# Kernel tuning notes

Hardware: AMD Instinct MI355X
Metric: run time of the kernel (lower is better)

The kernel has to match this reference:

```python
import jax, jax.numpy as jnp
import numpy as np

N_NODES = 2048


def setup_inputs() -> dict:
    key = jax.random.key(0)
    ks = jax.random.split(key, 9)
    N, IN, HID, OUT, R, B1 = N_NODES, 64, 32, 16, 4, 1
    s = 0.1
    return {
        "x": jax.random.normal(ks[0], (N, IN), jnp.float32),
        # adj_initial = ones - eye, as in __init__ (learnable parameter)
        "adj_matrix": jnp.ones((N, N), jnp.float32) - jnp.eye(N, dtype=jnp.float32),
        "bases1": jax.random.normal(ks[1], (B1, IN, HID), jnp.float32) * s,
        "coeff1": jax.random.normal(ks[2], (R, B1), jnp.float32) * s,
        "loop_w1": jax.random.normal(ks[3], (IN, HID), jnp.float32) * s,
        "bias1": jnp.zeros((HID,), jnp.float32),
        "bases2": jax.random.normal(ks[4], (R, HID, OUT), jnp.float32) * s,
        "coeff2": jax.random.normal(ks[5], (R, R), jnp.float32) * s,
        "loop_w2": jax.random.normal(ks[6], (HID, OUT), jnp.float32) * s,
        "bias2": jnp.zeros((OUT,), jnp.float32),
        "edge_type": 0,  # ignored by the module (etype is rebuilt as zeros)
    }


def _rel_graph_conv(h, bases, coeff, loop_w, bias, src, dst, n_nodes, act):
    # basis regularizer: W_r = sum_b coeff[r, b] * bases[b]; all edges have etype 0
    W0 = jnp.einsum('b,bio->io', coeff[0], bases)          # [in, out]
    msg = (h @ W0)[src]                                    # [E, out] gather-by-edge
    agg = jax.ops.segment_sum(msg, dst, num_segments=n_nodes)  # scatter-sum
    out = agg + h @ loop_w + bias                          # self-loop + bias
    return act(out)


def reference(x, adj_matrix, bases1, coeff1, loop_w1, bias1,
              bases2, coeff2, loop_w2, bias2, edge_type):
    N = x.shape[0]
    # sigmoid(adj_matrix) > 0 everywhere (sigmoid(0)=0.5 on the diagonal), so
    # torch.nonzero yields ALL N^2 pairs in row-major order: complete graph
    # with self-loops. Structure is static -> build edges with arange.
    idx = jnp.arange(N)
    src = jnp.repeat(idx, N)   # [N*N]
    dst = jnp.tile(idx, N)     # [N*N]
    h = _rel_graph_conv(x, bases1, coeff1, loop_w1, bias1, src, dst, N, jax.nn.relu)
    h = _rel_graph_conv(h, bases2, coeff2, loop_w2, bias2, src, dst, N, lambda z: z)
    return h
```

## Files before the change

kernel.cpp:

```cpp
#include <hip/hip_runtime.h>

#define NN   2048
#define IN   64
#define HID  32
#define OUTD 16

#define S0P 0
#define S1P 4096

__global__ __launch_bounds__(256) void k1_colsum_x(const float* __restrict__ x,
                                                   float* __restrict__ ws) {
    __shared__ float red[256];
    const int tid = threadIdx.x, b = blockIdx.x;
    const int col = tid & 63, grp = tid >> 6;
    const float* xb = x + b * 32 * IN;
    float s = 0.f;
#pragma unroll
    for (int r = 0; r < 8; ++r)
        s += xb[(grp * 8 + r) * IN + col];
    red[tid] = s;
    __syncthreads();
    if (tid < 64)
        ws[S0P + b * 64 + tid] = red[tid] + red[tid + 64] + red[tid + 128] + red[tid + 192];
}

__global__ __launch_bounds__(256) void k2_layer1(const float* __restrict__ x,
                                                 const float* __restrict__ bases1,
                                                 const float* __restrict__ coeff1,
                                                 const float* __restrict__ loop_w1,
                                                 const float* __restrict__ bias1,
                                                 const float* __restrict__ loop_w2,
                                                 float* __restrict__ ws,
                                                 float* __restrict__ out) {
    __shared__ float w1sh[IN * HID];
    __shared__ float xsh[32 * IN];
    __shared__ float w2sh[HID * OUTD];
    __shared__ float h1sh[32 * 33];
    __shared__ float s0sh[IN];
    __shared__ float agg1sh[HID];
    __shared__ float red[256];
    const int tid = threadIdx.x, b = blockIdx.x;

    const float4* x4  = (const float4*)(x + b * 32 * IN);
    const float4* w14 = (const float4*)loop_w1;
    float4 xa = x4[tid], xb4 = x4[tid + 256];
    float4 wa = w14[tid], wb = w14[tid + 256];
    float4 w2v = {0.f, 0.f, 0.f, 0.f};
    if (tid < 128) w2v = ((const float4*)loop_w2)[tid];

    {
        const int col = tid & 63, g = tid >> 6;
        float a0 = 0.f, a1 = 0.f, a2 = 0.f, a3 = 0.f;
#pragma unroll
        for (int k = 0; k < 4; ++k) {
            a0 += ws[S0P + (g * 16 + k     ) * 64 + col];
            a1 += ws[S0P + (g * 16 + 4 + k ) * 64 + col];
            a2 += ws[S0P + (g * 16 + 8 + k ) * 64 + col];
            a3 += ws[S0P + (g * 16 + 12 + k) * 64 + col];
        }
        ((float4*)xsh)[tid] = xa; ((float4*)xsh)[tid + 256] = xb4;
        ((float4*)w1sh)[tid] = wa; ((float4*)w1sh)[tid + 256] = wb;
        if (tid < 128) ((float4*)w2sh)[tid] = w2v;
        red[tid] = a0 + a1 + a2 + a3;
    }
    __syncthreads();
    if (tid < 64)
        s0sh[tid] = red[tid] + red[tid + 64] + red[tid + 128] + red[tid + 192];
    __syncthreads();

    {
        const int h = tid & 31, seg = tid >> 5;
        float p = 0.f;
#pragma unroll
        for (int k = 0; k < 8; ++k)
            p += s0sh[seg * 8 + k] * bases1[(seg * 8 + k) * HID + h];
        red[tid] = p;
        __syncthreads();
        if (tid < HID) {
            float t = 0.f;
#pragma unroll
            for (int g = 0; g < 8; ++g) t += red[g * 32 + tid];
            agg1sh[tid] = bias1[tid] + coeff1[0] * t;
        }
    }
    __syncthreads();

    {
        const int h = tid & 31, rgrp = tid >> 5;
        const float agg1v = agg1sh[h];
        float a0 = agg1v, a1 = agg1v, a2 = agg1v, a3 = agg1v;
#pragma unroll
        for (int k = 0; k < IN; ++k) {
            const float w = w1sh[k * HID + h];
            a0 += xsh[(rgrp +  0) * IN + k] * w;
            a1 += xsh[(rgrp +  8) * IN + k] * w;
            a2 += xsh[(rgrp + 16) * IN + k] * w;
            a3 += xsh[(rgrp + 24) * IN + k] * w;
        }
        a0 = fmaxf(a0, 0.f); a1 = fmaxf(a1, 0.f);
        a2 = fmaxf(a2, 0.f); a3 = fmaxf(a3, 0.f);
        h1sh[(rgrp +  0) * 33 + h] = a0;
        h1sh[(rgrp +  8) * 33 + h] = a1;
        h1sh[(rgrp + 16) * 33 + h] = a2;
        h1sh[(rgrp + 24) * 33 + h] = a3;
        red[tid] = a0 + a1 + a2 + a3;
    }
    __syncthreads();
    if (tid < HID) {
        float t = 0.f;
#pragma unroll
        for (int g = 0; g < 8; ++g) t += red[g * 32 + tid];
        ws[S1P + b * HID + tid] = t;
    }
    {
        const int r0 = tid >> 4, o = tid & 15;
        float acc0 = 0.f, acc1 = 0.f;
#pragma unroll
        for (int h = 0; h < HID; ++h) {
            const float w = w2sh[h * OUTD + o];
            acc0 += h1sh[(r0     ) * 33 + h] * w;
            acc1 += h1sh[(r0 + 16) * 33 + h] * w;
        }
        out[b * 512 + tid]       = acc0;
        out[b * 512 + 256 + tid] = acc1;
    }
}

__global__ __launch_bounds__(256) void k3_finish(const float* __restrict__ bases2,
                                                 const float* __restrict__ coeff2,
                                                 const float* __restrict__ bias2,
                                                 const float* __restrict__ ws,
                                                 float* __restrict__ out) {
    __shared__ float w2csh[HID * OUTD];
    __shared__ float s1sh[HID];
    __shared__ float agg2sh[OUTD];
    __shared__ float red[256];
    const int tid = threadIdx.x, b = blockIdx.x;

    {
        const float c20 = coeff2[0], c21 = coeff2[1], c22 = coeff2[2], c23 = coeff2[3];
#pragma unroll
        for (int j = 0; j < 2; ++j) {
            const int i = tid + j * 256;
            w2csh[i] = c20 * bases2[i]        + c21 * bases2[512 + i] +
                       c22 * bases2[1024 + i] + c23 * bases2[1536 + i];
        }
    }
    {
        const int h = tid & 31, g = tid >> 5;
        float a0 = 0.f, a1 = 0.f;
#pragma unroll
        for (int k = 0; k < 4; ++k) {
            a0 += ws[S1P + (g * 8 + k    ) * HID + h];
            a1 += ws[S1P + (g * 8 + 4 + k) * HID + h];
        }
        red[tid] = a0 + a1;
    }
    __syncthreads();
    if (tid < HID) {
        float t = 0.f;
#pragma unroll
        for (int g = 0; g < 8; ++g) t += red[g * 32 + tid];
        s1sh[tid] = t;
    }
    __syncthreads();
    if (tid < OUTD) {
        float s = 0.f;
#pragma unroll
        for (int h = 0; h < HID; ++h) s += s1sh[h] * w2csh[h * OUTD + tid];
        agg2sh[tid] = bias2[tid] + s;
    }
    __syncthreads();

    if (tid < 128) {
        const int i = b * 128 + tid;
        float4 v = ((float4*)out)[i];
        const int c = (tid & 3) << 2;
        v.x += agg2sh[c];     v.y += agg2sh[c + 1];
        v.z += agg2sh[c + 2]; v.w += agg2sh[c + 3];
        ((float4*)out)[i] = v;
    }
}

extern "C" void kernel_launch(void* const* d_in, const int* in_sizes, int n_in,
                              void* d_out, int out_size, void* d_ws, size_t ws_size,
                              hipStream_t stream) {
    const float* x       = (const float*)d_in[0];
    const float* bases1  = (const float*)d_in[2];
    const float* coeff1  = (const float*)d_in[3];
    const float* loop_w1 = (const float*)d_in[4];
    const float* bias1   = (const float*)d_in[5];
    const float* bases2  = (const float*)d_in[6];
    const float* coeff2  = (const float*)d_in[7];
    const float* loop_w2 = (const float*)d_in[8];
    const float* bias2   = (const float*)d_in[9];
    float* out = (float*)d_out;
    float* ws  = (float*)d_ws;

    k1_colsum_x<<<64, 256, 0, stream>>>(x, ws);
    k2_layer1 <<<64, 256, 0, stream>>>(x, bases1, coeff1, loop_w1, bias1, loop_w2, ws, out);
    k3_finish <<<64, 256, 0, stream>>>(bases2, coeff2, bias2, ws, out);
}
```

Before: 88.35 us.

## Fuse three kernels into one with grid-wide flag barriers

Merges the column-sum, layer-1 and finishing kernels into one kernel of 64 blocks. Cross-block dependencies are handled by spin-wait barriers on per-block flags in the workspace, which are reset inside the kernel for the next call. Each block keeps its layer-2 self-loop result in registers and adds the aggregate before a single store, so the output is no longer written and then re-read. The goal is to remove two kernel launches and the gaps between them. In exchange it depends on all 64 blocks being resident at once and on the flag words not already holding the magic value before the first call.

```diff
diff --git a/kernel.cpp b/kernel.cpp
--- a/kernel.cpp
+++ b/kernel.cpp
@@ -7,46 +7,89 @@
 
 #define S0P 0
 #define S1P 4096
-
-__global__ __launch_bounds__(256) void k1_colsum_x(const float* __restrict__ x,
-                                                   float* __restrict__ ws) {
-    __shared__ float red[256];
+#define F0W 6144
+#define F1W 6208
+#define MAGIC 0x3C0FFEE1u
+
+__global__ __launch_bounds__(256) void k_fused(const float* __restrict__ x,
+                                               const float* __restrict__ bases1,
+                                               const float* __restrict__ coeff1,
+                                               const float* __restrict__ loop_w1,
+                                               const float* __restrict__ bias1,
+                                               const float* __restrict__ bases2,
+                                               const float* __restrict__ coeff2,
+                                               const float* __restrict__ loop_w2,
+                                               const float* __restrict__ bias2,
+                                               float* __restrict__ ws,
+                                               float* __restrict__ out) {
+    __shared__ float  xsh[32 * IN];
+    __shared__ float  w1sh[IN * HID];
+    __shared__ float  b1sh[IN * HID];
+    __shared__ float  w2sh[HID * OUTD];
+    __shared__ float  w2csh[HID * OUTD];
+    __shared__ float  h1sh[32 * 33];
+    __shared__ float4 red4[256];
+    __shared__ float  red[256];
+    __shared__ float  s0sh[IN];
+    __shared__ float  agg1sh[HID];
+    __shared__ float  s1sh[HID];
+    __shared__ float  agg2sh[OUTD];
     const int tid = threadIdx.x, b = blockIdx.x;
-    const int col = tid & 63, grp = tid >> 6;
-    const float* xb = x + b * 32 * IN;
-    float s = 0.f;
-#pragma unroll
-    for (int r = 0; r < 8; ++r)
-        s += xb[(grp * 8 + r) * IN + col];
-    red[tid] = s;
-    __syncthreads();
-    if (tid < 64)
-        ws[S0P + b * 64 + tid] = red[tid] + red[tid + 64] + red[tid + 128] + red[tid + 192];
-}
-
-__global__ __launch_bounds__(256) void k2_layer1(const float* __restrict__ x,
-                                                 const float* __restrict__ bases1,
-                                                 const float* __restrict__ coeff1,
-                                                 const float* __restrict__ loop_w1,
-                                                 const float* __restrict__ bias1,
-                                                 const float* __restrict__ loop_w2,
-                                                 float* __restrict__ ws,
-                                                 float* __restrict__ out) {
-    __shared__ float w1sh[IN * HID];
-    __shared__ float xsh[32 * IN];
-    __shared__ float w2sh[HID * OUTD];
-    __shared__ float h1sh[32 * 33];
-    __shared__ float s0sh[IN];
-    __shared__ float agg1sh[HID];
-    __shared__ float red[256];
-    const int tid = threadIdx.x, b = blockIdx.x;
+    uint32_t* f0 = (uint32_t*)ws + F0W;
+    uint32_t* f1 = (uint32_t*)ws + F1W;
+
+    if (tid == 0)
+        __hip_atomic_store(&f1[b], 0u, __ATOMIC_RELAXED, __HIP_MEMORY_SCOPE_AGENT);
 
     const float4* x4  = (const float4*)(x + b * 32 * IN);
     const float4* w14 = (const float4*)loop_w1;
-    float4 xa = x4[tid], xb4 = x4[tid + 256];
+    const float4* b14 = (const float4*)bases1;
+    float4 xa = x4[tid], xb = x4[tid + 256];
     float4 wa = w14[tid], wb = w14[tid + 256];
+    float4 ba = b14[tid], bb = b14[tid + 256];
     float4 w2v = {0.f, 0.f, 0.f, 0.f};
     if (tid < 128) w2v = ((const float4*)loop_w2)[tid];
+
+    ((float4*)xsh)[tid]  = xa; ((float4*)xsh)[tid + 256]  = xb;
+    ((float4*)w1sh)[tid] = wa; ((float4*)w1sh)[tid + 256] = wb;
+    ((float4*)b1sh)[tid] = ba; ((float4*)b1sh)[tid + 256] = bb;
+    if (tid < 128) ((float4*)w2sh)[tid] = w2v;
+    {
+        const float c20 = coeff2[0], c21 = coeff2[1], c22 = coeff2[2], c23 = coeff2[3];
+#pragma unroll
+        for (int j = 0; j < 2; ++j) {
+            const int i = tid + j * 256;
+            w2csh[i] = c20 * bases2[i]        + c21 * bases2[512 + i] +
+                       c22 * bases2[1024 + i] + c23 * bases2[1536 + i];
+        }
+    }
+
+    {
+        float4 p;
+        p.x = xa.x + xb.x; p.y = xa.y + xb.y; p.z = xa.z + xb.z; p.w = xa.w + xb.w;
+        red4[tid] = p;
+    }
+    __syncthreads();
+    if (tid < 16) {
+        float4 t = {0.f, 0.f, 0.f, 0.f};
+#pragma unroll
+        for (int r = 0; r < 16; ++r) {
+            float4 v = red4[r * 16 + tid];
+            t.x += v.x; t.y += v.y; t.z += v.z; t.w += v.w;
+        }
+        ((float4*)(ws + S0P + b * 64))[tid] = t;
+    }
+    __syncthreads();
+    __threadfence();
+    if (tid == 0)
+        __hip_atomic_store(&f0[b], MAGIC, __ATOMIC_RELAXED, __HIP_MEMORY_SCOPE_AGENT);
+
+    if (tid < 64)
+        while (__hip_atomic_load(&f0[tid], __ATOMIC_RELAXED,
+                                 __HIP_MEMORY_SCOPE_AGENT) != MAGIC)
+            __builtin_amdgcn_s_sleep(1);
+    __syncthreads();
+    __threadfence();
 
     {
         const int col = tid & 63, g = tid >> 6;
@@ -58,9 +101,6 @@
             a2 += ws[S0P + (g * 16 + 8 + k ) * 64 + col];
             a3 += ws[S0P + (g * 16 + 12 + k) * 64 + col];
         }
-        ((float4*)xsh)[tid] = xa; ((float4*)xsh)[tid + 256] = xb4;
-        ((float4*)w1sh)[tid] = wa; ((float4*)w1sh)[tid + 256] = wb;
-        if (tid < 128) ((float4*)w2sh)[tid] = w2v;
         red[tid] = a0 + a1 + a2 + a3;
     }
     __syncthreads();
@@ -73,7 +113,7 @@
         float p = 0.f;
 #pragma unroll
         for (int k = 0; k < 8; ++k)
-            p += s0sh[seg * 8 + k] * bases1[(seg * 8 + k) * HID + h];
+            p += s0sh[seg * 8 + k] * b1sh[(seg * 8 + k) * HID + h];
         red[tid] = p;
         __syncthreads();
         if (tid < HID) {
@@ -112,40 +152,27 @@
         for (int g = 0; g < 8; ++g) t += red[g * 32 + tid];
         ws[S1P + b * HID + tid] = t;
     }
-    {
-        const int r0 = tid >> 4, o = tid & 15;
-        float acc0 = 0.f, acc1 = 0.f;
-#pragma unroll
-        for (int h = 0; h < HID; ++h) {
-            const float w = w2sh[h * OUTD + o];
-            acc0 += h1sh[(r0     ) * 33 + h] * w;
-            acc1 += h1sh[(r0 + 16) * 33 + h] * w;
-        }
-        out[b * 512 + tid]       = acc0;
-        out[b * 512 + 256 + tid] = acc1;
-    }
-}
-
-__global__ __launch_bounds__(256) void k3_finish(const float* __restrict__ bases2,
-                                                 const float* __restrict__ coeff2,
-                                                 const float* __restrict__ bias2,
-                                                 const float* __restrict__ ws,
-                                                 float* __restrict__ out) {
-    __shared__ float w2csh[HID * OUTD];
-    __shared__ float s1sh[HID];
-    __shared__ float agg2sh[OUTD];
-    __shared__ float red[256];
-    const int tid = threadIdx.x, b = blockIdx.x;
-
-    {
-        const float c20 = coeff2[0], c21 = coeff2[1], c22 = coeff2[2], c23 = coeff2[3];
-#pragma unroll
-        for (int j = 0; j < 2; ++j) {
-            const int i = tid + j * 256;
-            w2csh[i] = c20 * bases2[i]        + c21 * bases2[512 + i] +
-                       c22 * bases2[1024 + i] + c23 * bases2[1536 + i];
-        }
-    }
+    __syncthreads();
+    __threadfence();
+    if (tid == 0)
+        __hip_atomic_store(&f1[b], MAGIC, __ATOMIC_RELAXED, __HIP_MEMORY_SCOPE_AGENT);
+
+    const int r0 = tid >> 4, o = tid & 15;
+    float acc0 = 0.f, acc1 = 0.f;
+#pragma unroll
+    for (int h = 0; h < HID; ++h) {
+        const float w = w2sh[h * OUTD + o];
+        acc0 += h1sh[(r0     ) * 33 + h] * w;
+        acc1 += h1sh[(r0 + 16) * 33 + h] * w;
+    }
+
+    if (tid < 64)
+        while (__hip_atomic_load(&f1[tid], __ATOMIC_RELAXED,
+                                 __HIP_MEMORY_SCOPE_AGENT) != MAGIC)
+            __builtin_amdgcn_s_sleep(1);
+    __syncthreads();
+    __threadfence();
+
     {
         const int h = tid & 31, g = tid >> 5;
         float a0 = 0.f, a1 = 0.f;
@@ -172,14 +199,11 @@
     }
     __syncthreads();
 
-    if (tid < 128) {
-        const int i = b * 128 + tid;
-        float4 v = ((float4*)out)[i];
-        const int c = (tid & 3) << 2;
-        v.x += agg2sh[c];     v.y += agg2sh[c + 1];
-        v.z += agg2sh[c + 2]; v.w += agg2sh[c + 3];
-        ((float4*)out)[i] = v;
-    }
+    out[b * 512 + tid]       = acc0 + agg2sh[o];
+    out[b * 512 + 256 + tid] = acc1 + agg2sh[o];
+
+    if (tid == 0)
+        __hip_atomic_store(&f0[b], 0u, __ATOMIC_RELAXED, __HIP_MEMORY_SCOPE_AGENT);
 }
 
 extern "C" void kernel_launch(void* const* d_in, const int* in_sizes, int n_in,
@@ -197,7 +221,6 @@
     float* out = (float*)d_out;
     float* ws  = (float*)d_ws;
 
-    k1_colsum_x<<<64, 256, 0, stream>>>(x, ws);
-    k2_layer1 <<<64, 256, 0, stream>>>(x, bases1, coeff1, loop_w1, bias1, loop_w2, ws, out);
-    k3_finish <<<64, 256, 0, stream>>>(bases2, coeff2, bias2, ws, out);
+    k_fused<<<64, 256, 0, stream>>>(x, bases1, coeff1, loop_w1, bias1,
+                                    bases2, coeff2, loop_w2, bias2, ws, out);
 }
```

New measurement: 104.6 us. 18.4% more time.

## Fuse final bias-add kernel into layer1 via last-block atomic ticket

Applied to the files above, without the earlier changes.

Removes the third kernel launch by having each block of the layer-1 kernel increment an atomic ticket, with the last-arriving block reducing column sums and adding the layer-2 aggregate to the whole output. The ticket counter is reset in the first kernel. This saves a launch and its gap, but serializes the final 2048x16 output update onto a single block and adds fences and atomics.

```diff
diff --git a/kernel.cpp b/kernel.cpp
--- a/kernel.cpp
+++ b/kernel.cpp
@@ -7,11 +7,15 @@
 
 #define S0P 0
 #define S1P 4096
+#define TKT 6144
 
 __global__ __launch_bounds__(256) void k1_colsum_x(const float* __restrict__ x,
                                                    float* __restrict__ ws) {
     __shared__ float red[256];
     const int tid = threadIdx.x, b = blockIdx.x;
+    if (b == 0 && tid == 0)
+        __hip_atomic_store((uint32_t*)ws + TKT, 0u,
+                           __ATOMIC_RELAXED, __HIP_MEMORY_SCOPE_AGENT);
     const int col = tid & 63, grp = tid >> 6;
     const float* xb = x + b * 32 * IN;
     float s = 0.f;
@@ -24,22 +28,30 @@
         ws[S0P + b * 64 + tid] = red[tid] + red[tid + 64] + red[tid + 128] + red[tid + 192];
 }
 
-__global__ __launch_bounds__(256) void k2_layer1(const float* __restrict__ x,
-                                                 const float* __restrict__ bases1,
-                                                 const float* __restrict__ coeff1,
-                                                 const float* __restrict__ loop_w1,
-                                                 const float* __restrict__ bias1,
-                                                 const float* __restrict__ loop_w2,
-                                                 float* __restrict__ ws,
-                                                 float* __restrict__ out) {
+__global__ __launch_bounds__(256) void k2_fused(const float* __restrict__ x,
+                                                const float* __restrict__ bases1,
+                                                const float* __restrict__ coeff1,
+                                                const float* __restrict__ loop_w1,
+                                                const float* __restrict__ bias1,
+                                                const float* __restrict__ bases2,
+                                                const float* __restrict__ coeff2,
+                                                const float* __restrict__ loop_w2,
+                                                const float* __restrict__ bias2,
+                                                float* __restrict__ ws,
+                                                float* __restrict__ out) {
     __shared__ float w1sh[IN * HID];
     __shared__ float xsh[32 * IN];
     __shared__ float w2sh[HID * OUTD];
+    __shared__ float w2csh[HID * OUTD];
     __shared__ float h1sh[32 * 33];
     __shared__ float s0sh[IN];
     __shared__ float agg1sh[HID];
+    __shared__ float s1sh[HID];
+    __shared__ float agg2sh[OUTD];
     __shared__ float red[256];
+    __shared__ uint32_t last_sh;
     const int tid = threadIdx.x, b = blockIdx.x;
+    uint32_t* tkt = (uint32_t*)ws + TKT;
 
     const float4* x4  = (const float4*)(x + b * 32 * IN);
     const float4* w14 = (const float4*)loop_w1;
@@ -47,6 +59,15 @@
     float4 wa = w14[tid], wb = w14[tid + 256];
     float4 w2v = {0.f, 0.f, 0.f, 0.f};
     if (tid < 128) w2v = ((const float4*)loop_w2)[tid];
+    {
+        const float c20 = coeff2[0], c21 = coeff2[1], c22 = coeff2[2], c23 = coeff2[3];
+#pragma unroll
+        for (int j = 0; j < 2; ++j) {
+            const int i = tid + j * 256;
+            w2csh[i] = c20 * bases2[i]        + c21 * bases2[512 + i] +
+                       c22 * bases2[1024 + i] + c23 * bases2[1536 + i];
+        }
+    }
 
     {
         const int col = tid & 63, g = tid >> 6;
@@ -124,28 +145,18 @@
         out[b * 512 + tid]       = acc0;
         out[b * 512 + 256 + tid] = acc1;
     }
-}
-
-__global__ __launch_bounds__(256) void k3_finish(const float* __restrict__ bases2,
-                                                 const float* __restrict__ coeff2,
-                                                 const float* __restrict__ bias2,
-                                                 const float* __restrict__ ws,
-                                                 float* __restrict__ out) {
-    __shared__ float w2csh[HID * OUTD];
-    __shared__ float s1sh[HID];
-    __shared__ float agg2sh[OUTD];
-    __shared__ float red[256];
-    const int tid = threadIdx.x, b = blockIdx.x;
-
-    {
-        const float c20 = coeff2[0], c21 = coeff2[1], c22 = coeff2[2], c23 = coeff2[3];
-#pragma unroll
-        for (int j = 0; j < 2; ++j) {
-            const int i = tid + j * 256;
-            w2csh[i] = c20 * bases2[i]        + c21 * bases2[512 + i] +
-                       c22 * bases2[1024 + i] + c23 * bases2[1536 + i];
-        }
-    }
+
+    __syncthreads();
+    if (tid == 0) {
+        __threadfence();
+        const uint32_t old = __hip_atomic_fetch_add(tkt, 1u, __ATOMIC_ACQ_REL,
+                                                    __HIP_MEMORY_SCOPE_AGENT);
+        last_sh = (old == 63u);
+    }
+    __syncthreads();
+    if (!last_sh) return;
+    __threadfence();
+
     {
         const int h = tid & 31, g = tid >> 5;
         float a0 = 0.f, a1 = 0.f;
@@ -172,13 +183,16 @@
     }
     __syncthreads();
 
-    if (tid < 128) {
-        const int i = b * 128 + tid;
-        float4 v = ((float4*)out)[i];
+    {
+        float4* o4 = (float4*)out;
         const int c = (tid & 3) << 2;
-        v.x += agg2sh[c];     v.y += agg2sh[c + 1];
-        v.z += agg2sh[c + 2]; v.w += agg2sh[c + 3];
-        ((float4*)out)[i] = v;
+        const float4 av = { agg2sh[c], agg2sh[c + 1], agg2sh[c + 2], agg2sh[c + 3] };
+#pragma unroll 8
+        for (int j = 0; j < 32; ++j) {
+            float4 v = o4[j * 256 + tid];
+            v.x += av.x; v.y += av.y; v.z += av.z; v.w += av.w;
+            o4[j * 256 + tid] = v;
+        }
     }
 }
 
@@ -198,6 +212,6 @@
     float* ws  = (float*)d_ws;
 
     k1_colsum_x<<<64, 256, 0, stream>>>(x, ws);
-    k2_layer1 <<<64, 256, 0, stream>>>(x, bases1, coeff1, loop_w1, bias1, loop_w2, ws, out);
-    k3_finish <<<64, 256, 0, stream>>>(bases2, coeff2, bias2, ws, out);
+    k2_fused  <<<64, 256, 0, stream>>>(x, bases1, coeff1, loop_w1, bias1,
+                                       bases2, coeff2, loop_w2, bias2, ws, out);
 }
```

Result: slower. 97.05 us (+9.9%).
